# Kernel tuning notes

Measured on AMD Instinct MI355X. Metric: run time of the kernel, lower is better.

Reference implementation:

```python
import jax, jax.numpy as jnp
import numpy as np

NUM_HEADS = 16
NUM_KV_HEADS = 4
HEAD_DIM = 64
ROPE_BASE = 10000.0


def _rope(x, pos0):
    # x: [b, s, n, h_d]; interleaved-pair RoPE (torchtune RotaryPositionalEmbeddings)
    b, s, n, hd = x.shape
    half = hd // 2
    inv_freq = 1.0 / (ROPE_BASE ** (jnp.arange(0, hd, 2, dtype=jnp.float32) / hd))  # [half]
    t = jnp.arange(s, dtype=jnp.float32) + pos0                                      # [s]
    freqs = t[:, None] * inv_freq[None, :]                                           # [s, half]
    cos = jnp.cos(freqs)[None, :, None, :].astype(x.dtype)
    sin = jnp.sin(freqs)[None, :, None, :].astype(x.dtype)
    xr = x.reshape(b, s, n, half, 2)
    x1, x2 = xr[..., 0], xr[..., 1]
    o1 = x1 * cos - x2 * sin
    o2 = x1 * sin + x2 * cos
    return jnp.stack([o1, o2], axis=-1).reshape(b, s, n, hd)


def setup_inputs() -> dict:
    key = jax.random.key(0)
    k1, k2, k3 = jax.random.split(key, 3)
    b, s, d = 2, 2048, 1024
    qkv_dim = (NUM_HEADS + 2 * NUM_KV_HEADS) * HEAD_DIM  # 1536
    x = jax.random.normal(k1, (b, s, d), dtype=jnp.float32)
    Wqkv = jax.random.normal(k2, (d, qkv_dim), dtype=jnp.float32) * (d ** -0.5)
    Wo = jax.random.normal(k3, (d, d), dtype=jnp.float32) * (d ** -0.5)
    return {"x": x, "Wqkv": Wqkv, "Wo": Wo, "curr_pos": 0}


def reference(x, Wqkv, Wo, curr_pos):
    b, s, d = x.shape
    n_h, n_kv, hd = NUM_HEADS, NUM_KV_HEADS, HEAD_DIM
    q_per_kv = n_h // n_kv
    total_qkv = q_per_kv + 2

    # fused QKV projection then split per kv group
    qkv = (x @ Wqkv).reshape(b, s, n_kv, total_qkv, hd)
    q = qkv[:, :, :, :q_per_kv]            # [b, s, n_kv, q_per_kv, hd]
    k = qkv[:, :, :, q_per_kv:q_per_kv + 1]  # [b, s, n_kv, 1, hd]
    v = qkv[:, :, :, q_per_kv + 1:]          # [b, s, n_kv, 1, hd]

    # GQA expand k/v to match query heads, then flatten heads
    k = jnp.broadcast_to(k, (b, s, n_kv, q_per_kv, hd))
    v = jnp.broadcast_to(v, (b, s, n_kv, q_per_kv, hd))
    q = q.reshape(b, s, n_h, hd)
    k = k.reshape(b, s, n_h, hd)
    v = v.reshape(b, s, n_h, hd)

    # RoPE on q and k
    q = _rope(q, curr_pos)
    k = _rope(k, curr_pos)

    # causal SDPA (kv_cache is None -> is_causal=True, mask=None, dropout=0)
    scale = 1.0 / jnp.sqrt(jnp.asarray(hd, dtype=x.dtype))
    scores = jnp.einsum('bqhd,bkhd->bhqk', q, k) * scale  # [b, n_h, s, s]
    causal = jnp.tril(jnp.ones((s, s), dtype=bool))
    scores = jnp.where(causal[None, None], scores, jnp.finfo(scores.dtype).min)
    attn = jax.nn.softmax(scores, axis=-1)
    out = jnp.einsum('bhqk,bkhd->bqhd', attn, v).reshape(b, s, n_h * hd)
    return out @ Wo
```

## Files before the change

### kernel.cpp

```cpp
#include <hip/hip_runtime.h>
#include <hip/hip_bf16.h>

typedef __attribute__((ext_vector_type(8))) short bf16x8;
typedef __attribute__((ext_vector_type(4))) short bf16x4;
typedef __attribute__((ext_vector_type(4))) float f32x4;
typedef unsigned short u16;
typedef unsigned int u32;

#define NH 16
#define NKV 4
#define HD 64
#define BB 2
#define SS 2048
#define DD 1024
#define QKVD 1536

#define QSCALE 0.18033688011112f
#define MBIAS  -12.0f

template<bool B> struct BoolC { static constexpr bool value = B; };
template<int V>  struct IntC  { static constexpr int value = V; };

__device__ __forceinline__ u16 f2b(float f){
  __hip_bfloat16 h = __float2bfloat16(f);
  u16 u; __builtin_memcpy(&u, &h, 2); return u;
}
__device__ __forceinline__ float b2f(u32 u){
  u <<= 16; float f; __builtin_memcpy(&f, &u, 4); return f;
}
__device__ __forceinline__ float exp2fast(float x){
#if __has_builtin(__builtin_amdgcn_exp2f)
  return __builtin_amdgcn_exp2f(x);
#else
  return exp2f(x);
#endif
}

__device__ __forceinline__ void gload16(const void* g, void* l){
  __builtin_amdgcn_global_load_lds((const __attribute__((address_space(1))) void*)g,
                                   (__attribute__((address_space(3))) void*)l, 16, 0, 0);
}

__device__ __forceinline__ f32x4 mfma16(bf16x4 a, bf16x4 b, f32x4 c){
#if __has_builtin(__builtin_amdgcn_mfma_f32_16x16x16bf16_1k)
  return __builtin_amdgcn_mfma_f32_16x16x16bf16_1k(a, b, c, 0, 0, 0);
#else
  asm volatile("v_mfma_f32_16x16x16_bf16 %0, %1, %2, %0" : "+v"(c) : "v"(a), "v"(b));
  return c;
#endif
}

__global__ __launch_bounds__(256) void prep1(const float* __restrict__ x,
                                             u16* __restrict__ Xb,
                                             const float* __restrict__ Wqkv,
                                             u16* __restrict__ WqkvT,
                                             const float* __restrict__ Wo,
                                             u16* __restrict__ WoT){
  __shared__ u16 tile[64][65];
  const int bid = blockIdx.x;
  if (bid < 4096){
    int idx = (bid * 256 + threadIdx.x) * 4;
    float4 v = *(const float4*)(x + idx);
    u32 lo = (u32)f2b(v.x) | ((u32)f2b(v.y) << 16);
    u32 hi = (u32)f2b(v.z) | ((u32)f2b(v.w) << 16);
    *(uint2*)(Xb + idx) = make_uint2(lo, hi);
    return;
  }
  const float* in; u16* outT; int K, N, n0, k0;
  if (bid < 4480){
    int id = bid - 4096; in = Wqkv; outT = WqkvT; K = 1024; N = 1536;
    n0 = (id % 24) * 64; k0 = (id / 24) * 64;
  } else {
    int id = bid - 4480; in = Wo; outT = WoT; K = 1024; N = 1024;
    n0 = (id % 16) * 64; k0 = (id / 16) * 64;
  }
  int cr = threadIdx.x >> 6, cc = threadIdx.x & 63;
#pragma unroll
  for (int rr = 0; rr < 16; rr++){
    int row = rr * 4 + cr;
    tile[row][cc] = f2b(in[(size_t)(k0 + row) * N + n0 + cc]);
  }
  __syncthreads();
#pragma unroll
  for (int rr = 0; rr < 16; rr++){
    int row = rr * 4 + cr;
    outT[(size_t)(n0 + row) * K + k0 + cc] = tile[cc][row];
  }
}

template<int TN, typename OT>
__global__ __launch_bounds__(256) void gemm_db(const __hip_bfloat16* __restrict__ A,
                                               const __hip_bfloat16* __restrict__ BT,
                                               OT* __restrict__ C,
                                               int M, int N, int K){
  constexpr int NW = TN / 32;
  constexpr int ABYTES = 128 * 128;
  constexpr int BBYTES = TN * 128;
  __shared__ __align__(16) char smem[2][ABYTES + BBYTES];
  const int ntn = N / TN;
  int bid = blockIdx.x;
  const int cpx = gridDim.x >> 3;
  bid = (bid & 7) * cpx + (bid >> 3);
  const int tm = bid / ntn, tn = bid % ntn;
  const int m0 = tm << 7, n0 = tn * TN;
  const int lane = threadIdx.x & 63, w = threadIdx.x >> 6;
  const int g = lane >> 4, i = lane & 15;
  const int wr = w >> 1, wc = w & 1;
  f32x4 acc[4][NW] = {};
  const int lrow = lane >> 3;
  const int lcol = ((lane & 7) ^ lrow) * 8;
  const __hip_bfloat16* ga = A  + (size_t)(m0 + w * 32 + lrow) * K + lcol;
  const __hip_bfloat16* gb = BT + (size_t)(n0 + w * 8 + lrow) * K + lcol;
  const int xr = (i & 7) << 4;

  auto stage = [&](int buf, int kt){
    char* As = smem[buf];
    char* Bs = As + ABYTES;
#pragma unroll
    for (int h = 0; h < 4; h++)
      gload16(ga + kt + (size_t)(h * 8) * K, As + w * 4096 + h * 1024);
#pragma unroll
    for (int h = 0; h < NW; h++)
      gload16(gb + kt + (size_t)(h * 32) * K, Bs + (h * 4 + w) * 1024);
  };

  stage(0, 0);
  asm volatile("s_waitcnt vmcnt(0)");
  __syncthreads();
  int cur = 0;
  for (int kt = 0; kt < K; kt += 64){
    if (kt + 64 < K) stage(cur ^ 1, kt + 64);
    const char* As = smem[cur];
    const char* Bs = As + ABYTES;
    bf16x8 af[2][4], bfr[2][NW];
#pragma unroll
    for (int kh = 0; kh < 2; kh++){
#pragma unroll
      for (int x = 0; x < 4; x++)
        af[kh][x] = *(const bf16x8*)(As + (wr * 64 + x * 16 + i) * 128 + ((kh * 64 + g * 16) ^ xr));
#pragma unroll
      for (int n = 0; n < NW; n++)
        bfr[kh][n] = *(const bf16x8*)(Bs + (wc * (TN / 2) + n * 16 + i) * 128 + ((kh * 64 + g * 16) ^ xr));
    }
    __builtin_amdgcn_s_setprio(1);
#pragma unroll
    for (int kh = 0; kh < 2; kh++)
#pragma unroll
      for (int mi = 0; mi < 4; mi++)
#pragma unroll
        for (int ni = 0; ni < NW; ni++)
          acc[mi][ni] = __builtin_amdgcn_mfma_f32_16x16x32_bf16(af[kh][mi], bfr[kh][ni], acc[mi][ni], 0, 0, 0);
    __builtin_amdgcn_s_setprio(0);
    asm volatile("s_waitcnt vmcnt(0)");
    __syncthreads();
    cur ^= 1;
  }
#pragma unroll
  for (int mi = 0; mi < 4; mi++)
#pragma unroll
    for (int ni = 0; ni < NW; ni++){
      size_t base = (size_t)(m0 + wr * 64 + mi * 16 + g * 4) * N + n0 + wc * (TN / 2) + ni * 16 + i;
#pragma unroll
      for (int r = 0; r < 4; r++){
        float v = acc[mi][ni][r];
        if constexpr (sizeof(OT) == 2) C[base + (size_t)r * N] = (OT)f2b(v);
        else                           C[base + (size_t)r * N] = v;
      }
    }
}

__global__ __launch_bounds__(256) void prep2(const u16* __restrict__ qkv,
                                             const int* __restrict__ posp,
                                             u16* __restrict__ Qr,
                                             u16* __restrict__ Kr,
                                             u16* __restrict__ Vt){
  __shared__ u16 tile[64][65];
  const int bid = blockIdx.x;
  if (bid < 10240){
    int bx = bid & 255, h20 = (bid >> 8) % 20, bi = bid / 5120;
    int t = bx * 256 + threadIdx.x;
    int p = t & 31, si = t >> 5;
    int kvh = h20 / 5, slot = h20 - kvh * 5;
    const u16* src = qkv + (size_t)(bi * SS + si) * QKVD + (kvh * 6 + slot) * 64 + 2 * p;
    u32 pair = *(const u32*)src;
    float x1 = b2f(pair & 0xffffu), x2 = b2f(pair >> 16);
    int pos0 = posp[0];
    float inv_freq = exp2fast(-(float)p * 0.4152410118609203f);
    float ang = (float)(si + pos0) * inv_freq;
    float sn, cs;
    sincosf(ang, &sn, &cs);
    float o1 = x1 * cs - x2 * sn;
    float o2 = x1 * sn + x2 * cs;
    u16* dst;
    if (slot == 4){
      dst = Kr + ((size_t)(bi * NKV + kvh) * SS + si) * 64 + 2 * p;
    } else {
      o1 *= QSCALE; o2 *= QSCALE;
      dst = Qr + ((size_t)(bi * NH + kvh * 4 + slot) * SS + si) * 64 + 2 * p;
    }
    *(u32*)dst = (u32)f2b(o1) | ((u32)f2b(o2) << 16);
    return;
  }
  int id2 = bid - 10240;
  int st0 = (id2 & 31) * 64;
  int bkv = id2 >> 5;
  int bi = bkv >> 2, kvh = bkv & 3;
  int cr = threadIdx.x >> 6, cc = threadIdx.x & 63;
  const u16* src = qkv + (size_t)(bi * SS + st0) * QKVD + (kvh * 6 + 5) * 64;
#pragma unroll
  for (int rr = 0; rr < 16; rr++){
    int row = rr * 4 + cr;
    tile[row][cc] = src[(size_t)row * QKVD + cc];
  }
  __syncthreads();
  u16* dst = Vt + (size_t)bkv * 64 * SS + st0;
#pragma unroll
  for (int rr = 0; rr < 16; rr++){
    int row = rr * 4 + cr;
    dst[(size_t)row * SS + cc] = tile[cc][row];
  }
}

__global__ __launch_bounds__(512) void attn_fwd(const __hip_bfloat16* __restrict__ Qr,
                                                const __hip_bfloat16* __restrict__ Kr,
                                                const __hip_bfloat16* __restrict__ Vt,
                                                u16* __restrict__ Ao){
  __shared__ __align__(16) char smem[3 * 16384];
  const int blk = blockIdx.x;
  const int qt = 15 - (blk >> 5);
  const int bh = blk & 31;
  const int hi = bh & 15;
  const int bi = bh >> 4;
  const int kvh = hi >> 2;
  const int tid = threadIdx.x;
  const int lane = tid & 63, w = tid >> 6;
  const int g = lane >> 4, i = lane & 15;
  const int q0 = qt * 128 + w * 16;
  const u16* Qp = (const u16*)Qr + (size_t)(bi * NH + hi) * SS * 64;
  const u16* Kp = (const u16*)Kr + (size_t)(bi * NKV + kvh) * SS * 64;
  const u16* Vp = (const u16*)Vt + (size_t)(bi * NKV + kvh) * 64 * SS;
  bf16x8 qf0 = *(const bf16x8*)(Qp + (size_t)(q0 + i) * 64 + g * 8);
  bf16x8 qf1 = *(const bf16x8*)(Qp + (size_t)(q0 + i) * 64 + 32 + g * 8);

  const int srow = tid >> 3;
  const int sw   = ((tid & 7) ^ (srow & 7)) * 8;
  const int xr   = (i & 7) << 4;

  auto stage = [&](int buf, int j0){
    gload16(Kp + (size_t)(j0 + srow) * 64 + sw, &smem[buf * 16384 + w * 1024]);
    gload16(Vp + (size_t)srow * SS + j0 + sw,   &smem[buf * 16384 + 8192 + w * 1024]);
  };

  float l_row = 0.f;
  f32x4 o[4] = {};
  const int wlim = w * 16 + i;

  auto body = [&](auto modec, int buf){
    constexpr int MODE = decltype(modec)::value;
    if constexpr (MODE == 2){ if (w < 4) return; }
    const char* Kb = &smem[buf * 16384];
    const char* Vb = Kb + 8192;
    f32x4 st[4];
    __builtin_amdgcn_s_setprio(1);
#pragma unroll
    for (int jb = 0; jb < 4; jb++){
      const int row = jb * 16 + i;
      bf16x8 kf0 = *(const bf16x8*)(Kb + row * 128 + ((g * 16) ^ xr));
      bf16x8 kf1 = *(const bf16x8*)(Kb + row * 128 + ((64 + g * 16) ^ xr));
      f32x4 a = {MBIAS, MBIAS, MBIAS, MBIAS};
      a = __builtin_amdgcn_mfma_f32_16x16x32_bf16(kf0, qf0, a, 0, 0, 0);
      a = __builtin_amdgcn_mfma_f32_16x16x32_bf16(kf1, qf1, a, 0, 0, 0);
      st[jb] = a;
    }
    __builtin_amdgcn_s_setprio(0);
    bf16x4 vt[4][4];
#pragma unroll
    for (int db = 0; db < 4; db++){
      const int row = db * 16 + i;
#pragma unroll
      for (int mk = 0; mk < 4; mk++)
        vt[db][mk] = *(const bf16x4*)(Vb + row * 128 + ((mk * 32 + g * 8) ^ xr));
    }
    auto smpv = [&](auto diagc, int wl){
      constexpr bool DIAG = decltype(diagc)::value;
      float p[4][4];
#pragma unroll
      for (int jb = 0; jb < 4; jb++)
#pragma unroll
        for (int r = 0; r < 4; r++){
          float e = exp2fast(st[jb][r]);
          if constexpr (DIAG) e = (jb * 16 + g * 4 + r > wl) ? 0.f : e;
          p[jb][r] = e;
        }
      float sj[4];
#pragma unroll
      for (int jb = 0; jb < 4; jb++)
        sj[jb] = (p[jb][0] + p[jb][1]) + (p[jb][2] + p[jb][3]);
      float lsum = (sj[0] + sj[1]) + (sj[2] + sj[3]);
      lsum += __shfl_xor(lsum, 16, 64);
      lsum += __shfl_xor(lsum, 32, 64);
      l_row += lsum;
      __builtin_amdgcn_s_setprio(1);
#pragma unroll
      for (int mk = 0; mk < 4; mk++){
        bf16x4 pa;
#pragma unroll
        for (int r = 0; r < 4; r++) pa[r] = (short)f2b(p[mk][r]);
#pragma unroll
        for (int db = 0; db < 4; db++)
          o[db] = mfma16(vt[db][mk], pa, o[db]);
      }
      __builtin_amdgcn_s_setprio(0);
    };
    if constexpr (MODE == 0){
      smpv(BoolC<false>{}, 0);
    } else if constexpr (MODE == 1){
      if (w < 4) smpv(BoolC<true>{}, wlim);
      else       smpv(BoolC<false>{}, 0);
    } else {
      smpv(BoolC<true>{}, wlim - 64);
    }
  };

  const int nfull = 2 * qt;
  stage(0, 0);
  stage(1, 64);
  for (int t = 0; t < nfull; t++){
    asm volatile("s_waitcnt vmcnt(2)" ::: "memory");
    __builtin_amdgcn_s_barrier();
    asm volatile("" ::: "memory");
    stage((t + 2) % 3, (t + 2) * 64);
    body(IntC<0>{}, t % 3);
  }
  asm volatile("s_waitcnt vmcnt(2)" ::: "memory");
  __builtin_amdgcn_s_barrier();
  asm volatile("" ::: "memory");
  body(IntC<1>{}, nfull % 3);
  asm volatile("s_waitcnt vmcnt(0)" ::: "memory");
  __builtin_amdgcn_s_barrier();
  asm volatile("" ::: "memory");
  body(IntC<2>{}, (nfull + 1) % 3);

  const float linv = 1.f / l_row;
  u16* orow = Ao + (size_t)(bi * SS + q0 + i) * (NH * HD) + hi * 64 + g * 4;
#pragma unroll
  for (int db = 0; db < 4; db++){
    bf16x4 ov;
#pragma unroll
    for (int r = 0; r < 4; r++) ov[r] = (short)f2b(o[db][r] * linv);
    *(bf16x4*)(orow + db * 16) = ov;
  }
}

extern "C" void kernel_launch(void* const* d_in, const int* in_sizes, int n_in,
                              void* d_out, int out_size, void* d_ws, size_t ws_size,
                              hipStream_t stream){
  const float* x    = (const float*)d_in[0];
  const float* Wqkv = (const float*)d_in[1];
  const float* Wo   = (const float*)d_in[2];
  const int*   pos  = (const int*)d_in[3];
  float* out = (float*)d_out;
  char* ws = (char*)d_ws;

  __hip_bfloat16* Xb    = (__hip_bfloat16*)(ws);
  __hip_bfloat16* WqkvT = (__hip_bfloat16*)(ws + 8388608);
  __hip_bfloat16* WoT   = (__hip_bfloat16*)(ws + 11534336);
  u16*            QKVb  = (u16*)(ws + 13631488);
  __hip_bfloat16* Qr    = (__hip_bfloat16*)(ws + 26214400);
  __hip_bfloat16* Kr    = (__hip_bfloat16*)(ws + 34603008);
  __hip_bfloat16* Vt    = (__hip_bfloat16*)(ws + 36700160);
  __hip_bfloat16* Ao    = (__hip_bfloat16*)(ws);

  prep1<<<4736, 256, 0, stream>>>(x, (u16*)Xb, Wqkv, (u16*)WqkvT, Wo, (u16*)WoT);
  gemm_db<96, u16><<<512, 256, 0, stream>>>(Xb, WqkvT, QKVb, 4096, 1536, 1024);
  prep2<<<10496, 256, 0, stream>>>(QKVb, pos, (u16*)Qr, (u16*)Kr, (u16*)Vt);
  attn_fwd<<<512, 512, 0, stream>>>(Qr, Kr, Vt, (u16*)Ao);
  gemm_db<64, float><<<512, 256, 0, stream>>>(Ao, WoT, out, 4096, 1024, 1024);
}
```

Before: 92.30 us.

## Load K/V straight to registers in attention, dropping the LDS triple buffer

Attention no longer stages K/V tiles into shared memory with a barrier-synchronized triple buffer. Each wave now loads its own 32-key K and V fragments from global memory directly into registers, double-buffered so the next tile loads while the current one is computed. Blocks shrink to 256 threads with twice as many blocks, and each wave stops at its own causal limit instead of the block's. This removes LDS traffic and block-wide barriers, but waves sharing a head now fetch the same K/V separately, which relies on L2/L1 and raises global load traffic and register pressure.

```diff
diff --git a/kernel.cpp b/kernel.cpp
--- a/kernel.cpp
+++ b/kernel.cpp
@@ -19,7 +19,6 @@
 #define MBIAS  -12.0f
 
 template<bool B> struct BoolC { static constexpr bool value = B; };
-template<int V>  struct IntC  { static constexpr int value = V; };
 
 __device__ __forceinline__ u16 f2b(float f){
   __hip_bfloat16 h = __float2bfloat16(f);
@@ -221,125 +220,104 @@
   }
 }
 
-__global__ __launch_bounds__(512) void attn_fwd(const __hip_bfloat16* __restrict__ Qr,
+__global__ __launch_bounds__(256) void attn_fwd(const __hip_bfloat16* __restrict__ Qr,
                                                 const __hip_bfloat16* __restrict__ Kr,
                                                 const __hip_bfloat16* __restrict__ Vt,
                                                 u16* __restrict__ Ao){
-  __shared__ __align__(16) char smem[3 * 16384];
   const int blk = blockIdx.x;
-  const int qt = 15 - (blk >> 5);
-  const int bh = blk & 31;
+  const int qt = 15 - (blk >> 6);
+  const int rem = blk & 63;
+  const int half = rem >> 5;
+  const int bh = rem & 31;
   const int hi = bh & 15;
   const int bi = bh >> 4;
   const int kvh = hi >> 2;
-  const int tid = threadIdx.x;
-  const int lane = tid & 63, w = tid >> 6;
+  const int lane = threadIdx.x & 63, w = threadIdx.x >> 6;
   const int g = lane >> 4, i = lane & 15;
-  const int q0 = qt * 128 + w * 16;
+  const int ww = half * 4 + w;
+  const int q0 = qt * 128 + ww * 16;
+  const int qi = q0 + i;
   const u16* Qp = (const u16*)Qr + (size_t)(bi * NH + hi) * SS * 64;
   const u16* Kp = (const u16*)Kr + (size_t)(bi * NKV + kvh) * SS * 64;
   const u16* Vp = (const u16*)Vt + (size_t)(bi * NKV + kvh) * 64 * SS;
   bf16x8 qf0 = *(const bf16x8*)(Qp + (size_t)(q0 + i) * 64 + g * 8);
   bf16x8 qf1 = *(const bf16x8*)(Qp + (size_t)(q0 + i) * 64 + 32 + g * 8);
 
-  const int srow = tid >> 3;
-  const int sw   = ((tid & 7) ^ (srow & 7)) * 8;
-  const int xr   = (i & 7) << 4;
-
-  auto stage = [&](int buf, int j0){
-    gload16(Kp + (size_t)(j0 + srow) * 64 + sw, &smem[buf * 16384 + w * 1024]);
-    gload16(Vp + (size_t)srow * SS + j0 + sw,   &smem[buf * 16384 + 8192 + w * 1024]);
-  };
-
   float l_row = 0.f;
   f32x4 o[4] = {};
-  const int wlim = w * 16 + i;
-
-  auto body = [&](auto modec, int buf){
-    constexpr int MODE = decltype(modec)::value;
-    if constexpr (MODE == 2){ if (w < 4) return; }
-    const char* Kb = &smem[buf * 16384];
-    const char* Vb = Kb + 8192;
-    f32x4 st[4];
+
+  auto ldkv = [&](bf16x8 (&kc)[4], bf16x4 (&vc)[8], int j0){
+#pragma unroll
+    for (int jb = 0; jb < 2; jb++){
+      const u16* kp = Kp + (size_t)(j0 + jb * 16 + i) * 64 + g * 8;
+      kc[jb * 2 + 0] = *(const bf16x8*)kp;
+      kc[jb * 2 + 1] = *(const bf16x8*)(kp + 32);
+    }
+#pragma unroll
+    for (int db = 0; db < 4; db++){
+      const u16* vp = Vp + (size_t)(db * 16 + i) * SS + j0 + g * 4;
+      vc[db * 2 + 0] = *(const bf16x4*)vp;
+      vc[db * 2 + 1] = *(const bf16x4*)(vp + 16);
+    }
+  };
+
+  auto cmp = [&](const bf16x8 (&kc)[4], const bf16x4 (&vc)[8], int j0, auto diagc){
+    constexpr bool DIAG = decltype(diagc)::value;
+    f32x4 st[2];
     __builtin_amdgcn_s_setprio(1);
 #pragma unroll
-    for (int jb = 0; jb < 4; jb++){
-      const int row = jb * 16 + i;
-      bf16x8 kf0 = *(const bf16x8*)(Kb + row * 128 + ((g * 16) ^ xr));
-      bf16x8 kf1 = *(const bf16x8*)(Kb + row * 128 + ((64 + g * 16) ^ xr));
+    for (int jb = 0; jb < 2; jb++){
       f32x4 a = {MBIAS, MBIAS, MBIAS, MBIAS};
-      a = __builtin_amdgcn_mfma_f32_16x16x32_bf16(kf0, qf0, a, 0, 0, 0);
-      a = __builtin_amdgcn_mfma_f32_16x16x32_bf16(kf1, qf1, a, 0, 0, 0);
+      a = __builtin_amdgcn_mfma_f32_16x16x32_bf16(kc[jb * 2 + 0], qf0, a, 0, 0, 0);
+      a = __builtin_amdgcn_mfma_f32_16x16x32_bf16(kc[jb * 2 + 1], qf1, a, 0, 0, 0);
       st[jb] = a;
     }
     __builtin_amdgcn_s_setprio(0);
-    bf16x4 vt[4][4];
-#pragma unroll
-    for (int db = 0; db < 4; db++){
-      const int row = db * 16 + i;
-#pragma unroll
-      for (int mk = 0; mk < 4; mk++)
-        vt[db][mk] = *(const bf16x4*)(Vb + row * 128 + ((mk * 32 + g * 8) ^ xr));
-    }
-    auto smpv = [&](auto diagc, int wl){
-      constexpr bool DIAG = decltype(diagc)::value;
-      float p[4][4];
-#pragma unroll
-      for (int jb = 0; jb < 4; jb++)
-#pragma unroll
-        for (int r = 0; r < 4; r++){
-          float e = exp2fast(st[jb][r]);
-          if constexpr (DIAG) e = (jb * 16 + g * 4 + r > wl) ? 0.f : e;
-          p[jb][r] = e;
-        }
-      float sj[4];
-#pragma unroll
-      for (int jb = 0; jb < 4; jb++)
-        sj[jb] = (p[jb][0] + p[jb][1]) + (p[jb][2] + p[jb][3]);
-      float lsum = (sj[0] + sj[1]) + (sj[2] + sj[3]);
-      lsum += __shfl_xor(lsum, 16, 64);
-      lsum += __shfl_xor(lsum, 32, 64);
-      l_row += lsum;
-      __builtin_amdgcn_s_setprio(1);
-#pragma unroll
-      for (int mk = 0; mk < 4; mk++){
-        bf16x4 pa;
-#pragma unroll
-        for (int r = 0; r < 4; r++) pa[r] = (short)f2b(p[mk][r]);
-#pragma unroll
-        for (int db = 0; db < 4; db++)
-          o[db] = mfma16(vt[db][mk], pa, o[db]);
+    float p[2][4];
+#pragma unroll
+    for (int jb = 0; jb < 2; jb++)
+#pragma unroll
+      for (int r = 0; r < 4; r++){
+        float e = exp2fast(st[jb][r]);
+        if constexpr (DIAG) e = (j0 + jb * 16 + g * 4 + r > qi) ? 0.f : e;
+        p[jb][r] = e;
       }
-      __builtin_amdgcn_s_setprio(0);
-    };
-    if constexpr (MODE == 0){
-      smpv(BoolC<false>{}, 0);
-    } else if constexpr (MODE == 1){
-      if (w < 4) smpv(BoolC<true>{}, wlim);
-      else       smpv(BoolC<false>{}, 0);
-    } else {
-      smpv(BoolC<true>{}, wlim - 64);
-    }
+    float lsum = ((p[0][0] + p[0][1]) + (p[0][2] + p[0][3]))
+               + ((p[1][0] + p[1][1]) + (p[1][2] + p[1][3]));
+    lsum += __shfl_xor(lsum, 16, 64);
+    lsum += __shfl_xor(lsum, 32, 64);
+    l_row += lsum;
+    __builtin_amdgcn_s_setprio(1);
+#pragma unroll
+    for (int mk = 0; mk < 2; mk++){
+      bf16x4 pa;
+#pragma unroll
+      for (int r = 0; r < 4; r++) pa[r] = (short)f2b(p[mk][r]);
+#pragma unroll
+      for (int db = 0; db < 4; db++)
+        o[db] = mfma16(vc[db * 2 + mk], pa, o[db]);
+    }
+    __builtin_amdgcn_s_setprio(0);
   };
 
-  const int nfull = 2 * qt;
-  stage(0, 0);
-  stage(1, 64);
-  for (int t = 0; t < nfull; t++){
-    asm volatile("s_waitcnt vmcnt(2)" ::: "memory");
-    __builtin_amdgcn_s_barrier();
-    asm volatile("" ::: "memory");
-    stage((t + 2) % 3, (t + 2) * 64);
-    body(IntC<0>{}, t % 3);
-  }
-  asm volatile("s_waitcnt vmcnt(2)" ::: "memory");
-  __builtin_amdgcn_s_barrier();
-  asm volatile("" ::: "memory");
-  body(IntC<1>{}, nfull % 3);
-  asm volatile("s_waitcnt vmcnt(0)" ::: "memory");
-  __builtin_amdgcn_s_barrier();
-  asm volatile("" ::: "memory");
-  body(IntC<2>{}, (nfull + 1) % 3);
+  const int nfull = qt * 4 + (ww >> 1);
+  bf16x8 kA[4], kB[4];
+  bf16x4 vA[8], vB[8];
+  ldkv(kA, vA, 0);
+  int t = 0;
+  for (; t + 2 <= nfull; t += 2){
+    ldkv(kB, vB, (t + 1) * 32);
+    cmp(kA, vA, t * 32, BoolC<false>{});
+    ldkv(kA, vA, (t + 2) * 32);
+    cmp(kB, vB, (t + 1) * 32, BoolC<false>{});
+  }
+  if (t < nfull){
+    ldkv(kB, vB, (t + 1) * 32);
+    cmp(kA, vA, t * 32, BoolC<false>{});
+    cmp(kB, vB, (t + 1) * 32, BoolC<true>{});
+  } else {
+    cmp(kA, vA, t * 32, BoolC<true>{});
+  }
 
   const float linv = 1.f / l_row;
   u16* orow = Ao + (size_t)(bi * SS + q0 + i) * (NH * HD) + hi * 64 + g * 4;
@@ -374,6 +352,6 @@
   prep1<<<4736, 256, 0, stream>>>(x, (u16*)Xb, Wqkv, (u16*)WqkvT, Wo, (u16*)WoT);
   gemm_db<96, u16><<<512, 256, 0, stream>>>(Xb, WqkvT, QKVb, 4096, 1536, 1024);
   prep2<<<10496, 256, 0, stream>>>(QKVb, pos, (u16*)Qr, (u16*)Kr, (u16*)Vt);
-  attn_fwd<<<512, 512, 0, stream>>>(Qr, Kr, Vt, (u16*)Ao);
+  attn_fwd<<<1024, 256, 0, stream>>>(Qr, Kr, Vt, (u16*)Ao);
   gemm_db<64, float><<<512, 256, 0, stream>>>(Ao, WoT, out, 4096, 1024, 1024);
 }
```

After: 241.8 us. 162% more time.
